# Optimization experiments

Measured on AMD Instinct MI355X. Metric: run time of the kernel, lower is better.

The kernel has to match this reference:

```python
import jax, jax.numpy as jnp
import numpy as np

G, N, K, F = 256, 512, 6, 64  # graphs, nodes/graph, knn k, n_features
T = G * N

def leaky(x):
    return jnp.where(x >= 0, x, 0.2 * x)

def prelu(x, a):
    return jnp.where(x >= 0, x, a * x)

def knn_idx(x):
    # per-graph kNN (k=6, self excluded); idx[i] = global indices of 6 nearest nbrs of i
    xg = x.reshape(G, N, F)
    sq = jnp.sum(xg * xg, axis=-1)                       # [G,N]
    d = sq[:, :, None] + sq[:, None, :] - 2.0 * jnp.einsum('gnf,gmf->gnm', xg, xg)
    d = jnp.where(jnp.eye(N, dtype=bool)[None], jnp.inf, d)  # loop=False
    _, idx = jax.lax.top_k(-d, K)                        # [G,N,K] local indices
    idx = idx + (jnp.arange(G) * N)[:, None, None]       # make global
    return idx.reshape(T, K)

def gconv(h, idx, W, b):
    # PyG GeneralConv defaults: out[i] = sum_{j in nbr(i)} (x_j W + b) + x_i
    s = jnp.take(h, idx, axis=0).sum(axis=1)             # [T,F] sum of neighbor feats
    return s @ W + K * b + h

def forward(x, W1, b1, a1, W2, b2, a2,
            Wc1, bc1, Wc2, bc2, Wc3, bc3, Wc4, bc4,
            W3, b3, a3, W4, b4, a4,
            Wh1, bh1, Wh2, bh2, Wh3, bh3, Wh4, bh4, idx):
    h = prelu(x @ W1 + b1, a1)
    h = prelu(h @ W2 + b2, a2)
    h = gconv(h, idx, Wc1, bc1)
    h = gconv(h, idx, Wc2, bc2)
    h = gconv(h, idx, Wc3, bc3)
    h = gconv(h, idx, Wc4, bc4)
    h = prelu(h @ W3 + b3, a3)
    h = prelu(h @ W4 + b4, a4)
    pooled = h.reshape(G, N, F).sum(axis=1)              # global_add_pool -> [G,F]
    y = leaky(pooled @ Wh1 + bh1)
    y = leaky(y @ Wh2 + bh2)
    y = leaky(y @ Wh3 + bh3)
    return y @ Wh4 + bh4                                 # [G,1]

def setup_inputs():
    key = jax.random.key(0)
    ks = jax.random.split(key, 16)
    def lin(k, i, o):
        k1, k2 = jax.random.split(k)
        s = 1.0 / np.sqrt(i)
        return (jax.random.uniform(k1, (i, o), jnp.float32, -s, s),
                jax.random.uniform(k2, (o,), jnp.float32, -s, s))
    inp = {"x": jax.random.normal(ks[0], (T, F), jnp.float32)}
    W1, b1 = lin(ks[1], F, F); W2, b2 = lin(ks[2], F, F)
    Wc1, bc1 = lin(ks[3], F, F); Wc2, bc2 = lin(ks[4], F, F)
    Wc3, bc3 = lin(ks[5], F, F); Wc4, bc4 = lin(ks[6], F, F)
    W3, b3 = lin(ks[7], F, F); W4, b4 = lin(ks[8], F, F)
    Wh1, bh1 = lin(ks[9], F, 4 * F); Wh2, bh2 = lin(ks[10], 4 * F, 4 * F)
    Wh3, bh3 = lin(ks[11], 4 * F, F); Wh4, bh4 = lin(ks[12], F, 1)
    a = 0.25 * jnp.ones((F,), jnp.float32)  # PReLU init
    inp.update(W1=W1, b1=b1, a1=a, W2=W2, b2=b2, a2=a,
               Wc1=Wc1, bc1=bc1, Wc2=Wc2, bc2=bc2, Wc3=Wc3, bc3=bc3, Wc4=Wc4, bc4=bc4,
               W3=W3, b3=b3, a3=a, W4=W4, b4=b4, a4=a,
               Wh1=Wh1, bh1=bh1, Wh2=Wh2, bh2=bh2, Wh3=Wh3, bh3=bh3, Wh4=Wh4, bh4=bh4)
    return inp

def reference(x, W1, b1, a1, W2, b2, a2, Wc1, bc1, Wc2, bc2, Wc3, bc3, Wc4, bc4,
              W3, b3, a3, W4, b4, a4, Wh1, bh1, Wh2, bh2, Wh3, bh3, Wh4, bh4):
    idx = knn_idx(x)  # edge_index built from raw x, as in the torch module
    return forward(x, W1, b1, a1, W2, b2, a2, Wc1, bc1, Wc2, bc2, Wc3, bc3, Wc4, bc4,
                   W3, b3, a3, W4, b4, a4, Wh1, bh1, Wh2, bh2, Wh3, bh3, Wh4, bh4, idx)
```

## Files before the change

### kernel.cpp

```cpp
#include <hip/hip_runtime.h>

#define NGRAPH 256
#define NNODE  512
#define KNN    6
#define NCAND  12
#define NF     64
#define SBF    72
#define NT     768
#define NW     12
#define PBF    18432
#define CANDO  PBF
#define SQO    (PBF + 3072)
#define WTO    36864
#define NBRO   39168
#define LDS_FLOATS 40704
#define LDS_BYTES  (LDS_FLOATS*4)
#define POOLP  PBF
#define POOLED (PBF + 1024)
#define Y1OFF  (PBF + 1088)
#define Y2OFF  (PBF + 1344)
#define BIG 1e30f

typedef float v4f __attribute__((ext_vector_type(4)));
typedef float v2f __attribute__((ext_vector_type(2)));
typedef short v8s __attribute__((ext_vector_type(8)));

struct Params {
  const float *x;
  const float *W1,*b1,*a1, *W2,*b2,*a2;
  const float *Wc0,*bc0, *Wc1,*bc1, *Wc2,*bc2, *Wc3,*bc3;
  const float *W3,*b3,*a3, *W4,*b4,*a4;
  const float *Wh1,*bh1, *Wh2,*bh2, *Wh3,*bh3, *Wh4,*bh4;
  float *out;
};

__device__ __forceinline__ unsigned f2bf(float x) {
  union { float f; unsigned u; } cc; cc.f = x;
  unsigned u = cc.u;
  return (u + 0x7FFFu + ((u >> 16) & 1u)) >> 16;
}
__device__ __forceinline__ float bflo(unsigned u) {
  union { unsigned u; float f; } c; c.u = u << 16; return c.f;
}
__device__ __forceinline__ float bfhi(unsigned u) {
  union { unsigned u; float f; } c; c.u = u & 0xffff0000u; return c.f;
}
__device__ __forceinline__ v2f up2(unsigned u) {
  v2f r; r.x = bflo(u); r.y = bfhi(u); return r;
}

__device__ __forceinline__ v8s bfrag(const unsigned short* base, int row, int c0) {
  return *(const v8s*)(base + row*SBF + c0);
}

__device__ __forceinline__ float packe(float e, int j) {
  return __uint_as_float((__float_as_uint(e) & 0xFFFFFE00u) | (unsigned)j);
}

__device__ __forceinline__ void ins8(float (&b)[8], float v) {
  if (v < b[7]) {
#pragma unroll
    for (int p = 0; p < 8; ++p) {
      float lo = fminf(b[p], v);
      v = fmaxf(b[p], v);
      b[p] = lo;
    }
  }
}
__device__ __forceinline__ void ins12(float (&b)[NCAND], float v) {
  if (v < b[NCAND-1]) {
#pragma unroll
    for (int p = 0; p < NCAND; ++p) {
      float lo = fminf(b[p], v);
      v = fmaxf(b[p], v);
      b[p] = lo;
    }
  }
}

__device__ __forceinline__ void ld8(const float* W, float (&wf)[8], int tid) {
  const int col = tid >> 3, ks = (tid & 7) * 8;
  const float* wp = W + col;
#pragma unroll
  for (int i = 0; i < 8; ++i) wf[i] = wp[(ks + i) * NF];
}
__device__ __forceinline__ void wt_write(const float (&wf)[8], unsigned short* wt, int tid) {
  const int col = tid >> 3, ks = (tid & 7) * 8;
  unsigned d[4];
#pragma unroll
  for (int i = 0; i < 4; ++i)
    d[i] = f2bf(wf[2*i]) | (f2bf(wf[2*i+1]) << 16);
  *(uint4*)&wt[col*SBF + ks] = make_uint4(d[0], d[1], d[2], d[3]);
}

template<int NTILE>
__device__ __forceinline__ void filter_tiles(const unsigned short* hbf,
                                             const float* ldsf,
                                             unsigned short* cand,
                                             const int (&tts)[NTILE],
                                             int lane, int c, int qq) {
  v8s A0[NTILE], A1[NTILE];
  float d8[NTILE][8];
  int i0[NTILE];
#pragma unroll
  for (int k = 0; k < NTILE; ++k) {
    i0[k] = tts[k] * 16;
    A0[k] = bfrag(hbf, i0[k] + c, qq*8);
    A1[k] = bfrag(hbf, i0[k] + c, 32 + qq*8);
#pragma unroll
    for (int m = 0; m < 8; ++m) d8[k][m] = BIG;
  }
#pragma unroll 1
  for (int jt = 0; jt < 32; ++jt) {
    const int j0 = jt * 16;
    v8s B0 = bfrag(hbf, j0 + c, qq*8);
    v8s B1 = bfrag(hbf, j0 + c, 32 + qq*8);
    float4 sv = *(const float4*)&ldsf[SQO + j0 + qq*4];
    const int jb = j0 + qq*4;
#pragma unroll
    for (int k = 0; k < NTILE; ++k) {
      v4f acc = {0.f, 0.f, 0.f, 0.f};
      acc = __builtin_amdgcn_mfma_f32_16x16x32_bf16(B0, A0[k], acc, 0, 0, 0);
      acc = __builtin_amdgcn_mfma_f32_16x16x32_bf16(B1, A1[k], acc, 0, 0, 0);
      float e0 = fmaf(-2.f, acc[0], sv.x);
      float e1 = fmaf(-2.f, acc[1], sv.y);
      float e2 = fmaf(-2.f, acc[2], sv.z);
      float e3 = fmaf(-2.f, acc[3], sv.w);
      if (jt == tts[k]) {
        const int myrow = i0[k] + c;
        if (jb     == myrow) e0 = BIG;
        if (jb + 1 == myrow) e1 = BIG;
        if (jb + 2 == myrow) e2 = BIG;
        if (jb + 3 == myrow) e3 = BIG;
      }
      ins8(d8[k], packe(e0, jb));
      ins8(d8[k], packe(e1, jb+1));
      ins8(d8[k], packe(e2, jb+2));
      ins8(d8[k], packe(e3, jb+3));
    }
  }
#pragma unroll
  for (int k = 0; k < NTILE; ++k) {
    float cd[NCAND];
#pragma unroll
    for (int m = 0; m < 8; ++m) cd[m] = d8[k][m];
#pragma unroll
    for (int m = 8; m < NCAND; ++m) cd[m] = BIG;
    {
      float pd[8];
#pragma unroll
      for (int s = 0; s < 8; ++s) pd[s] = __shfl_xor(cd[s], 16);
#pragma unroll
      for (int s = 0; s < 8; ++s) ins12(cd, pd[s]);
    }
    {
      float pd[NCAND];
#pragma unroll
      for (int s = 0; s < NCAND; ++s) pd[s] = __shfl_xor(cd[s], 32);
#pragma unroll
      for (int s = 0; s < NCAND; ++s) ins12(cd, pd[s]);
    }
    if (lane < 16) {
#pragma unroll
      for (int s = 0; s < NCAND; ++s)
        cand[(i0[k] + lane)*NCAND + s] =
          (unsigned short)(__float_as_uint(cd[s]) & 0x1FFu);
    }
  }
}

__global__ __launch_bounds__(NT) void fused_gnn(Params P) {
  extern __shared__ float lds[];
  unsigned short* hbf  = (unsigned short*)lds;
  unsigned short* pbf  = (unsigned short*)&lds[PBF];
  unsigned short* wt   = (unsigned short*)&lds[WTO];
  unsigned short* cand = (unsigned short*)&lds[CANDO];
  unsigned short* nbrs = (unsigned short*)&lds[NBRO];
  const int tid  = threadIdx.x;
  const int g    = blockIdx.x;
  const int rA   = tid;
  const int lane = tid & 63;
  const int w    = tid >> 6;
  const int c    = lane & 15;
  const int qq   = lane >> 4;

  const float* xgp = P.x + (size_t)g * NNODE * NF;
  const float4* xg = (const float4*)xgp;

#pragma unroll 1
  for (int i = tid; i < NNODE*NF/4; i += NT) {
    float4 v = xg[i];
    int row = i >> 4, k4 = i & 15;
    unsigned lo = f2bf(v.x) | (f2bf(v.y) << 16);
    unsigned hi = f2bf(v.z) | (f2bf(v.w) << 16);
    *(uint2*)&hbf[row*SBF + 4*k4] = make_uint2(lo, hi);
  }
  __syncthreads();

  if (tid < 512) {
    const uint4* xr = (const uint4*)(hbf + rA*SBF);
    float s = 0.f;
#pragma unroll
    for (int k = 0; k < 8; ++k) {
      uint4 u = xr[k];
      float f;
      f = bflo(u.x); s = fmaf(f, f, s); f = bfhi(u.x); s = fmaf(f, f, s);
      f = bflo(u.y); s = fmaf(f, f, s); f = bfhi(u.y); s = fmaf(f, f, s);
      f = bflo(u.z); s = fmaf(f, f, s); f = bfhi(u.z); s = fmaf(f, f, s);
      f = bflo(u.w); s = fmaf(f, f, s); f = bfhi(u.w); s = fmaf(f, f, s);
    }
    lds[SQO + rA] = s;
  }
  __syncthreads();

  if (w < 8) {
    int tts[3] = {w, w + 8, w + 16};
    filter_tiles<3>(hbf, lds, cand, tts, lane, c, qq);
  } else {
    int tts[2] = {w + 16, w + 20};
    filter_tiles<2>(hbf, lds, cand, tts, lane, c, qq);
  }
  __syncthreads();

  float4 xr16[16];
  if (tid < 512) {
    const float4* xrow = (const float4*)(xgp + rA*NF);
#pragma unroll
    for (int k4 = 0; k4 < 16; ++k4) xr16[k4] = xrow[k4];
    float s0 = 0.f;
#pragma unroll
    for (int k4 = 0; k4 < 16; ++k4) {
      float4 a = xr16[k4];
      s0 = fmaf(a.x,a.x,s0); s0 = fmaf(a.y,a.y,s0); s0 = fmaf(a.z,a.z,s0); s0 = fmaf(a.w,a.w,s0);
    }
    lds[SQO + rA] = s0;
  }
  __syncthreads();

  if (tid < 512) {
    float nd[6]; int ni[6];
#pragma unroll
    for (int m = 0; m < 6; ++m) { nd[m] = BIG; ni[m] = 0x7fffffff; }
    int cnd[NCAND];
#pragma unroll
    for (int s = 0; s < NCAND; ++s) cnd[s] = cand[rA*NCAND + s];

#pragma unroll 1
    for (int s = 0; s < NCAND; ++s) {
      int j = cnd[s];
      const float4* xj = (const float4*)(xgp + j*NF);
      float4 aa = {0.f, 0.f, 0.f, 0.f};
#pragma unroll
      for (int k4 = 0; k4 < 16; ++k4) {
        float4 v = xj[k4];
        aa.x = fmaf(xr16[k4].x, v.x, aa.x); aa.y = fmaf(xr16[k4].y, v.y, aa.y);
        aa.z = fmaf(xr16[k4].z, v.z, aa.z); aa.w = fmaf(xr16[k4].w, v.w, aa.w);
      }
      float e = fmaf(-2.f, (aa.x+aa.y)+(aa.z+aa.w), lds[SQO + j]);
      if (e < nd[5] || (e == nd[5] && j < ni[5])) {
#pragma unroll
        for (int pp = 0; pp < 6; ++pp) {
          bool lt = (e < nd[pp]) || (e == nd[pp] && j < ni[pp]);
          float tb2 = nd[pp]; int ti = ni[pp];
          nd[pp] = lt ? e : tb2;  ni[pp] = lt ? j : ti;
          e      = lt ? tb2 : e;  j      = lt ? ti : j;
        }
      }
    }
#pragma unroll
    for (int m = 0; m < 6; ++m) nbrs[rA*KNN + m] = (unsigned short)ni[m];
  }

  float wf[8];
  if (tid < 512) ld8(P.W1, wf, tid);
  __syncthreads();
  if (tid < 512) { wt_write(wf, wt, tid); ld8(P.W2, wf, tid); }
  __syncthreads();

#pragma unroll 1
  for (int L = 0; L < 7; ++L) {
    const bool isconv = (L >= 2 && L <= 5);
    const float* bl = L==0?P.b1 : L==1?P.b2 : L==2?P.bc0 : L==3?P.bc1 :
                      L==4?P.bc2 : L==5?P.bc3 : P.b3;
    const float* al = L==0?P.a1 : L==1?P.a2 : P.a3;

    v8s B0[4], B1[4];
#pragma unroll
    for (int n = 0; n < 4; ++n) {
      B0[n] = bfrag(wt, n*16 + c, qq*8);
      B1[n] = bfrag(wt, n*16 + c, 32 + qq*8);
    }
    float br[4], ar[4];
    if (!isconv) {
#pragma unroll
      for (int n = 0; n < 4; ++n) { br[n] = bl[n*16 + c]; ar[n] = al[n*16 + c]; }
    }
    __syncthreads();

    if (tid < 512) {
      wt_write(wf, wt, tid);
      if (L < 6) {
        const float* Wn2 = L==0?P.Wc0 : L==1?P.Wc1 : L==2?P.Wc2 :
                           L==3?P.Wc3 : L==4?P.W3 : P.W4;
        ld8(Wn2, wf, tid);
      }
    }

#pragma unroll 1
    for (int tt = w; tt < 32; tt += NW) {
      const int i0 = tt * 16;
      v8s A0 = bfrag(hbf, i0 + c, qq*8);
      v8s A1 = bfrag(hbf, i0 + c, 32 + qq*8);
#pragma unroll
      for (int n = 0; n < 4; ++n) {
        v4f acc = {0.f, 0.f, 0.f, 0.f};
        acc = __builtin_amdgcn_mfma_f32_16x16x32_bf16(A0, B0[n], acc, 0, 0, 0);
        acc = __builtin_amdgcn_mfma_f32_16x16x32_bf16(A1, B1[n], acc, 0, 0, 0);
        if (isconv) {
#pragma unroll
          for (int r = 0; r < 4; ++r)
            pbf[(i0 + qq*4 + r)*SBF + n*16 + c] = (unsigned short)f2bf(acc[r]);
        } else {
#pragma unroll
          for (int r = 0; r < 4; ++r) {
            float v = acc[r] + br[n];
            v = v >= 0.f ? v : ar[n]*v;
            hbf[(i0 + qq*4 + r)*SBF + n*16 + c] = (unsigned short)f2bf(v);
          }
        }
      }
    }
    __syncthreads();

    if (isconv) {
      const int s = tid & 7;
      const float* bls = bl + 8*s;
      float4 bv0 = *(const float4*)(bls);
      float4 bv1 = *(const float4*)(bls + 4);
#pragma unroll 1
      for (int r = tid >> 3; r < NNODE; r += NT/8) {
        const unsigned short* nb = &nbrs[r*KNN];
        uint4 own = *(const uint4*)&hbf[r*SBF + 8*s];
        v2f a0 = up2(own.x), a1 = up2(own.y), a2 = up2(own.z), a3 = up2(own.w);
        v2f t;
        t.x = bv0.x; t.y = bv0.y; a0 += 6.f*t;
        t.x = bv0.z; t.y = bv0.w; a1 += 6.f*t;
        t.x = bv1.x; t.y = bv1.y; a2 += 6.f*t;
        t.x = bv1.z; t.y = bv1.w; a3 += 6.f*t;
#pragma unroll
        for (int mm = 0; mm < KNN; ++mm) {
          int nbr = nb[mm];
          uint4 p = *(const uint4*)&pbf[nbr*SBF + 8*s];
          a0 += up2(p.x); a1 += up2(p.y); a2 += up2(p.z); a3 += up2(p.w);
        }
        uint4 o;
        o.x = f2bf(a0.x) | (f2bf(a0.y) << 16);
        o.y = f2bf(a1.x) | (f2bf(a1.y) << 16);
        o.z = f2bf(a2.x) | (f2bf(a2.y) << 16);
        o.w = f2bf(a3.x) | (f2bf(a3.y) << 16);
        *(uint4*)&hbf[r*SBF + 8*s] = o;
      }
    }
  }

  {
    v8s B0[4], B1[4];
#pragma unroll
    for (int n = 0; n < 4; ++n) {
      B0[n] = bfrag(wt, n*16 + c, qq*8);
      B1[n] = bfrag(wt, n*16 + c, 32 + qq*8);
    }
    float br[4], ar[4];
#pragma unroll
    for (int n = 0; n < 4; ++n) { br[n] = P.b4[n*16 + c]; ar[n] = P.a4[n*16 + c]; }

    float ps[4] = {0.f, 0.f, 0.f, 0.f};
#pragma unroll 1
    for (int tt = w; tt < 32; tt += NW) {
      const int i0 = tt * 16;
      v8s A0 = bfrag(hbf, i0 + c, qq*8);
      v8s A1 = bfrag(hbf, i0 + c, 32 + qq*8);
#pragma unroll
      for (int n = 0; n < 4; ++n) {
        v4f acc = {0.f, 0.f, 0.f, 0.f};
        acc = __builtin_amdgcn_mfma_f32_16x16x32_bf16(A0, B0[n], acc, 0, 0, 0);
        acc = __builtin_amdgcn_mfma_f32_16x16x32_bf16(A1, B1[n], acc, 0, 0, 0);
#pragma unroll
        for (int r = 0; r < 4; ++r) {
          float v = acc[r] + br[n];
          v = v >= 0.f ? v : ar[n]*v;
          ps[n] += v;
        }
      }
    }
#pragma unroll
    for (int n = 0; n < 4; ++n) {
      ps[n] += __shfl_xor(ps[n], 16);
      ps[n] += __shfl_xor(ps[n], 32);
    }
    if (lane < 16) {
#pragma unroll
      for (int n = 0; n < 4; ++n) lds[POOLP + w*64 + n*16 + c] = ps[n];
    }
  }
  __syncthreads();

  if (tid < 64) {
    float pool = 0.f;
#pragma unroll
    for (int cc = 0; cc < NW; ++cc) pool += lds[POOLP + cc*64 + tid];
    lds[POOLED + tid] = pool;
  }
  __syncthreads();

  if (tid < 256) {
    float acc = P.bh1[tid];
#pragma unroll 4
    for (int k = 0; k < 64; ++k) acc = fmaf(lds[POOLED+k], P.Wh1[k*256 + tid], acc);
    lds[Y1OFF + tid] = acc >= 0.f ? acc : 0.2f*acc;
  }
  __syncthreads();
  if (tid < 512) {
    int o = tid & 255, hh = tid >> 8;
    float acc = hh ? 0.f : P.bh2[o];
    const int k0 = hh * 128;
#pragma unroll 4
    for (int k = k0; k < k0 + 128; ++k) acc = fmaf(lds[Y1OFF+k], P.Wh2[k*256 + o], acc);
    lds[POOLP + hh*256 + o] = acc;
  }
  __syncthreads();
  if (tid < 256) {
    float acc = lds[POOLP + tid] + lds[POOLP + 256 + tid];
    lds[Y2OFF + tid] = acc >= 0.f ? acc : 0.2f*acc;
  }
  __syncthreads();
  if (tid < 256) {
    int o = tid & 63, hh = tid >> 6;
    float acc = 0.f;
    const int k0 = hh * 64;
#pragma unroll 4
    for (int k = k0; k < k0 + 64; ++k) acc = fmaf(lds[Y2OFF+k], P.Wh3[k*64 + o], acc);
    lds[POOLP + hh*64 + o] = acc;
  }
  __syncthreads();
  if (tid < 64) {
    float acc = P.bh3[tid] + lds[POOLP + tid] + lds[POOLP + 64 + tid]
              + lds[POOLP + 128 + tid] + lds[POOLP + 192 + tid];
    float y3 = acc >= 0.f ? acc : 0.2f*acc;
    float v = y3 * P.Wh4[tid];
#pragma unroll
    for (int off = 32; off >= 1; off >>= 1) v += __shfl_down(v, off);
    if (tid == 0) P.out[g] = v + P.bh4[0];
  }
}

extern "C" void kernel_launch(void* const* d_in, const int* in_sizes, int n_in,
                              void* d_out, int out_size, void* d_ws, size_t ws_size,
                              hipStream_t stream) {
  Params P;
  P.x   = (const float*)d_in[0];
  P.W1  = (const float*)d_in[1];  P.b1  = (const float*)d_in[2];  P.a1 = (const float*)d_in[3];
  P.W2  = (const float*)d_in[4];  P.b2  = (const float*)d_in[5];  P.a2 = (const float*)d_in[6];
  P.Wc0 = (const float*)d_in[7];  P.bc0 = (const float*)d_in[8];
  P.Wc1 = (const float*)d_in[9];  P.bc1 = (const float*)d_in[10];
  P.Wc2 = (const float*)d_in[11]; P.bc2 = (const float*)d_in[12];
  P.Wc3 = (const float*)d_in[13]; P.bc3 = (const float*)d_in[14];
  P.W3  = (const float*)d_in[15]; P.b3  = (const float*)d_in[16]; P.a3 = (const float*)d_in[17];
  P.W4  = (const float*)d_in[18]; P.b4  = (const float*)d_in[19]; P.a4 = (const float*)d_in[20];
  P.Wh1 = (const float*)d_in[21]; P.bh1 = (const float*)d_in[22];
  P.Wh2 = (const float*)d_in[23]; P.bh2 = (const float*)d_in[24];
  P.Wh3 = (const float*)d_in[25]; P.bh3 = (const float*)d_in[26];
  P.Wh4 = (const float*)d_in[27]; P.bh4 = (const float*)d_in[28];
  P.out = (float*)d_out;

  (void)hipFuncSetAttribute(reinterpret_cast<const void*>(fused_gnn),
                            hipFuncAttributeMaxDynamicSharedMemorySize, LDS_BYTES);

  fused_gnn<<<NGRAPH, NT, LDS_BYTES, stream>>>(P);
}
```

Before: 297.3 us.

## Overlap first MLP layer on idle waves with kNN candidate refinement

Waves 8-11, which sat idle during the exact-distance top-6 refinement run by threads below 512, now compute layer 0 (x@W1+b1, PReLU) with MFMA and write it back to the bf16 feature buffer. W1 is staged earlier and W2/Wc0 are prefetched at the end of the refinement, which removes two barriers and one loop iteration from the layer loop. The refinement loop is also unrolled by two. This relies on the refinement reading raw x from global memory rather than hbf, so overwriting hbf at the same time is safe; it adds register pressure from the extra fragments held live.

```diff
diff --git a/kernel.cpp b/kernel.cpp
--- a/kernel.cpp
+++ b/kernel.cpp
@@ -220,9 +220,13 @@
     int tts[2] = {w + 16, w + 20};
     filter_tiles<2>(hbf, lds, cand, tts, lane, c, qq);
   }
+  float wf[8];
+  if (tid < 512) { ld8(P.W1, wf, tid); wt_write(wf, wt, tid); }
   __syncthreads();
 
   float4 xr16[16];
+  v8s LB0[4], LB1[4];
+  float lbr[4], lar[4];
   if (tid < 512) {
     const float4* xrow = (const float4*)(xgp + rA*NF);
 #pragma unroll
@@ -234,6 +238,14 @@
       s0 = fmaf(a.x,a.x,s0); s0 = fmaf(a.y,a.y,s0); s0 = fmaf(a.z,a.z,s0); s0 = fmaf(a.w,a.w,s0);
     }
     lds[SQO + rA] = s0;
+  } else {
+#pragma unroll
+    for (int n = 0; n < 4; ++n) {
+      LB0[n] = bfrag(wt, n*16 + c, qq*8);
+      LB1[n] = bfrag(wt, n*16 + c, 32 + qq*8);
+      lbr[n] = P.b1[n*16 + c];
+      lar[n] = P.a1[n*16 + c];
+    }
   }
   __syncthreads();
 
@@ -245,7 +257,7 @@
 #pragma unroll
     for (int s = 0; s < NCAND; ++s) cnd[s] = cand[rA*NCAND + s];
 
-#pragma unroll 1
+#pragma unroll 2
     for (int s = 0; s < NCAND; ++s) {
       int j = cnd[s];
       const float4* xj = (const float4*)(xgp + j*NF);
@@ -269,20 +281,37 @@
     }
 #pragma unroll
     for (int m = 0; m < 6; ++m) nbrs[rA*KNN + m] = (unsigned short)ni[m];
-  }
-
-  float wf[8];
-  if (tid < 512) ld8(P.W1, wf, tid);
-  __syncthreads();
-  if (tid < 512) { wt_write(wf, wt, tid); ld8(P.W2, wf, tid); }
-  __syncthreads();
-
-#pragma unroll 1
-  for (int L = 0; L < 7; ++L) {
+    ld8(P.W2, wf, tid);
+    wt_write(wf, wt, tid);
+    ld8(P.Wc0, wf, tid);
+  } else {
+#pragma unroll 1
+    for (int tt = w - 8; tt < 32; tt += 4) {
+      const int i0 = tt * 16;
+      v8s A0 = bfrag(hbf, i0 + c, qq*8);
+      v8s A1 = bfrag(hbf, i0 + c, 32 + qq*8);
+#pragma unroll
+      for (int n = 0; n < 4; ++n) {
+        v4f acc = {0.f, 0.f, 0.f, 0.f};
+        acc = __builtin_amdgcn_mfma_f32_16x16x32_bf16(A0, LB0[n], acc, 0, 0, 0);
+        acc = __builtin_amdgcn_mfma_f32_16x16x32_bf16(A1, LB1[n], acc, 0, 0, 0);
+#pragma unroll
+        for (int r = 0; r < 4; ++r) {
+          float v = acc[r] + lbr[n];
+          v = v >= 0.f ? v : lar[n]*v;
+          hbf[(i0 + qq*4 + r)*SBF + n*16 + c] = (unsigned short)f2bf(v);
+        }
+      }
+    }
+  }
+  __syncthreads();
+
+#pragma unroll 1
+  for (int L = 1; L < 7; ++L) {
     const bool isconv = (L >= 2 && L <= 5);
-    const float* bl = L==0?P.b1 : L==1?P.b2 : L==2?P.bc0 : L==3?P.bc1 :
+    const float* bl = L==1?P.b2 : L==2?P.bc0 : L==3?P.bc1 :
                       L==4?P.bc2 : L==5?P.bc3 : P.b3;
-    const float* al = L==0?P.a1 : L==1?P.a2 : P.a3;
+    const float* al = L==1?P.a2 : P.a3;
 
     v8s B0[4], B1[4];
 #pragma unroll
@@ -300,8 +329,8 @@
     if (tid < 512) {
       wt_write(wf, wt, tid);
       if (L < 6) {
-        const float* Wn2 = L==0?P.Wc0 : L==1?P.Wc1 : L==2?P.Wc2 :
-                           L==3?P.Wc3 : L==4?P.W3 : P.W4;
+        const float* Wn2 = L==1?P.Wc1 : L==2?P.Wc2 : L==3?P.Wc3 :
+                           L==4?P.W3 : P.W4;
         ld8(Wn2, wf, tid);
       }
     }
```

New measurement: 293.3 us. About the same (-1.4%).
